# Kernel tuning notes

Hardware: AMD Instinct MI355X
Metric: run time of the kernel (lower is better)

Reference implementation:

```python
import jax, jax.numpy as jnp
import numpy as np

N_NODES = 30000
N_EDGES = 300000
N_TRIP = 200000
NUM_RELS = 8
F_RAW = 128
D = 256  # rgcn_in_dim == h_dim


def setup_inputs() -> dict:
    key = jax.random.key(0)
    ks = jax.random.split(key, 14)
    feats = jax.random.normal(ks[0], (N_NODES, F_RAW), jnp.float32)
    src = jax.random.randint(ks[1], (N_EDGES,), 0, N_NODES)
    dst = jax.random.randint(ks[2], (N_EDGES,), 0, N_NODES)
    etype = jax.random.randint(ks[3], (N_EDGES,), 0, NUM_RELS)
    trip_s = jax.random.randint(ks[4], (N_TRIP,), 0, N_NODES)
    trip_r = jax.random.randint(ks[5], (N_TRIP,), 0, NUM_RELS)
    trip_o = jax.random.randint(ks[6], (N_TRIP,), 0, N_NODES)
    # learned parameters
    W_affine = jax.random.normal(ks[7], (F_RAW, D), jnp.float32) * (1.0 / np.sqrt(F_RAW))
    b_affine = jnp.zeros((D,), jnp.float32)
    W_fwd = jax.random.normal(ks[8], (NUM_RELS, D, D), jnp.float32) * (1.0 / np.sqrt(D))
    W_bwd = jax.random.normal(ks[9], (NUM_RELS, D, D), jnp.float32) * (1.0 / np.sqrt(D))
    W_loop = jax.random.normal(ks[10], (D, D), jnp.float32) * (1.0 / np.sqrt(D))
    w_relation = jax.random.normal(ks[11], (NUM_RELS, D), jnp.float32)  # nn.init.normal_(0,1)
    return {
        "feats": feats, "W_affine": W_affine, "b_affine": b_affine,
        "W_fwd": W_fwd, "W_bwd": W_bwd, "W_loop": W_loop,
        "w_relation": w_relation,
        "src": src, "dst": dst, "etype": etype,
        "trip_s": trip_s, "trip_r": trip_r, "trip_o": trip_o,
    }


def reference(feats, W_affine, b_affine, W_fwd, W_bwd, W_loop, w_relation,
              src, dst, etype, trip_s, trip_r, trip_o):
    # LinearAffine: raw features -> rgcn_in_dim
    x = feats @ W_affine + b_affine                      # [N, D]
    n = x.shape[0]
    # Per-relation transforms of all node features: [R, N, D]
    tf = jnp.einsum('ni,rio->rno', x, W_fwd)
    tb = jnp.einsum('ni,rio->rno', x, W_bwd)
    # Forward-direction messages: gather per-edge transformed src, scatter-add to dst
    msg_f = tf[etype, src]                               # [E, D]
    agg = jnp.zeros((n, x.shape[1]), x.dtype).at[dst].add(msg_f)
    # Backward-direction messages: transformed dst features scattered to src
    msg_b = tb[etype, dst]                               # [E, D]
    agg = agg.at[src].add(msg_b)
    # Self-loop
    h = agg + x @ W_loop                                 # [N, D]
    # DistMult triplet scoring
    s = h[trip_s]
    r = w_relation[trip_r]
    o = h[trip_o]
    weights = jnp.sum(s * r * o, axis=1)                 # [T]
    return weights, h
```

## Files before the change

### kernel.cpp

```cpp
#include <hip/hip_runtime.h>

#define N_NODES 30000
#define N_EDGES 300000
#define N_TRIP 200000
#define NUM_RELS 8
#define F_RAW 128
#define DDIM 256

#define NBUCK (2 * NUM_RELS * N_NODES)
#define SCAN_CHUNK 1024
#define NCHUNK ((NBUCK + SCAN_CHUNK - 1) / SCAN_CHUNK)
#define NPAD (NCHUNK * SCAN_CHUNK)

#define KBIG 2304
#define KBWD 2048
#define KMRG 4352

typedef __attribute__((ext_vector_type(8))) short short8;
typedef __attribute__((ext_vector_type(4))) float f32x4;

__device__ inline unsigned short f2bf(float f) {
  unsigned u = __builtin_bit_cast(unsigned, f);
  u = (u + 0x7FFFu + ((u >> 16) & 1u)) >> 16;
  return (unsigned short)u;
}
__device__ inline float bf2f(unsigned short s) {
  unsigned u = ((unsigned)s) << 16;
  return __builtin_bit_cast(float, u);
}

__global__ void zero_int_kernel(int* __restrict__ p, int n) {
  int i = blockIdx.x * blockDim.x + threadIdx.x;
  if (i < n) p[i] = 0;
}

__global__ void hist_kernel(const int* __restrict__ src,
                            const int* __restrict__ dst,
                            const int* __restrict__ et, int* __restrict__ cnt) {
  int e = blockIdx.x * blockDim.x + threadIdx.x;
  if (e >= N_EDGES) return;
  int r = et[e];
  atomicAdd(&cnt[r * N_NODES + dst[e]], 1);
  atomicAdd(&cnt[(NUM_RELS + r) * N_NODES + src[e]], 1);
}

__global__ __launch_bounds__(256) void scan1_kernel(const int* __restrict__ cnt,
                                                    int* __restrict__ offs,
                                                    int* __restrict__ bsum) {
  __shared__ int s[256];
  const int b = blockIdx.x, t = threadIdx.x;
  const int base = b * SCAN_CHUNK + t * 4;
  int4 v = *reinterpret_cast<const int4*>(&cnt[base]);
  int tsum = v.x + v.y + v.z + v.w;
  s[t] = tsum;
  __syncthreads();
  for (int off = 1; off < 256; off <<= 1) {
    int x = (t >= off) ? s[t - off] : 0;
    __syncthreads();
    s[t] += x;
    __syncthreads();
  }
  int excl = s[t] - tsum;
  offs[base + 0] = excl;
  offs[base + 1] = excl + v.x;
  offs[base + 2] = excl + v.x + v.y;
  offs[base + 3] = excl + v.x + v.y + v.z;
  if (t == 0) bsum[b] = s[255];
}

__global__ __launch_bounds__(512) void scan2_kernel(int* __restrict__ bsum) {
  __shared__ int s[512];
  const int t = threadIdx.x;
  int v = (t < NCHUNK) ? bsum[t] : 0;
  s[t] = v;
  __syncthreads();
  for (int off = 1; off < 512; off <<= 1) {
    int x = (t >= off) ? s[t - off] : 0;
    __syncthreads();
    s[t] += x;
    __syncthreads();
  }
  if (t < NCHUNK) bsum[t] = s[t] - v;
}

__global__ void scan3_kernel(int* __restrict__ offs,
                             const int* __restrict__ bsum,
                             int* __restrict__ cur) {
  int i = blockIdx.x * blockDim.x + threadIdx.x;
  if (i >= NPAD) return;
  int v = offs[i] + bsum[i / SCAN_CHUNK];
  offs[i] = v;
  if (i < NBUCK) cur[i] = v;
}

__global__ void fill_kernel(const int* __restrict__ src,
                            const int* __restrict__ dst,
                            const int* __restrict__ et, int* __restrict__ cur,
                            int* __restrict__ gidx) {
  int e = blockIdx.x * blockDim.x + threadIdx.x;
  if (e >= N_EDGES) return;
  int r = et[e];
  int s = src[e], d = dst[e];
  int p1 = atomicAdd(&cur[r * N_NODES + d], 1);
  gidx[p1] = s;
  int p2 = atomicAdd(&cur[(NUM_RELS + r) * N_NODES + s], 1);
  gidx[p2] = d;
}

__global__ void convert_bf16_kernel(const float* __restrict__ src,
                                    unsigned short* __restrict__ dst,
                                    int total) {
  const int i = blockIdx.x * blockDim.x + threadIdx.x;
  if (i < total) dst[i] = f2bf(src[i]);
}

__global__ void transpose_bf16_kernel(const float* __restrict__ src,
                                      unsigned short* __restrict__ dst,
                                      int R, int K, int N) {
  const int i = blockIdx.x * blockDim.x + threadIdx.x;
  const int total = R * K * N;
  if (i >= total) return;
  const int r = i / (K * N);
  const int rem = i - r * K * N;
  const int k = rem / N;
  const int n = rem - k * N;
  dst[(size_t)r * K * N + (size_t)n * K + k] = f2bf(src[i]);
}

__global__ void build_wcat2_kernel(const float* __restrict__ W8,
                                   const float* __restrict__ Wextra,
                                   unsigned short* __restrict__ dst, int KK) {
  const int i = blockIdx.x * blockDim.x + threadIdx.x;
  if (i >= 256 * KK) return;
  const int n = i / KK;
  const int kk = i - n * KK;
  float v;
  if (kk < 2048) {
    const int r = kk >> 8, k = kk & 255;
    v = W8[((size_t)r * 256 + k) * 256 + n];
  } else {
    v = Wextra[(size_t)(kk - 2048) * 256 + n];
  }
  dst[i] = f2bf(v);
}

__global__ void build_wcat3_kernel(const float* __restrict__ Wf,
                                   const float* __restrict__ Wb,
                                   const float* __restrict__ Wl,
                                   unsigned short* __restrict__ dst) {
  const int i = blockIdx.x * blockDim.x + threadIdx.x;
  if (i >= 256 * KMRG) return;
  const int n = i / KMRG;
  const int kk = i - n * KMRG;
  float v;
  if (kk < 2048) {
    const int r = kk >> 8, k = kk & 255;
    v = Wf[((size_t)r * 256 + k) * 256 + n];
  } else if (kk < 4096) {
    const int r = (kk - 2048) >> 8, k = kk & 255;
    v = Wb[((size_t)r * 256 + k) * 256 + n];
  } else {
    v = Wl[(size_t)(kk - 4096) * 256 + n];
  }
  dst[i] = f2bf(v);
}

template <int OUT_MODE, int ADD_BIAS>
__global__ __launch_bounds__(256) void gemm128_kernel(
    const unsigned short* __restrict__ A, int lda, int K,
    const unsigned short* __restrict__ Bt, const float* __restrict__ bias,
    float* __restrict__ Cf, unsigned short* __restrict__ Cb, int ldc, int M) {
  __shared__ __align__(16) unsigned short As[128 * 64];
  __shared__ __align__(16) unsigned short Bs[128 * 64];

  const int tid = threadIdx.x;
  const int lane = tid & 63;
  const int wave = tid >> 6;
  const int bm = blockIdx.y * 128;
  const int bn = blockIdx.x * 128;
  const int wr = wave >> 1;
  const int wc = wave & 1;
  const int g = lane >> 4;
  const int rl = lane & 15;

  f32x4 acc[4][4];
#pragma unroll
  for (int i = 0; i < 4; ++i)
#pragma unroll
    for (int j = 0; j < 4; ++j) acc[i][j] = (f32x4){0.f, 0.f, 0.f, 0.f};

  for (int k0 = 0; k0 < K; k0 += 64) {
#pragma unroll
    for (int c = 0; c < 8; ++c) {
      const int chunk = c * 4 + wave;
      if (chunk < 16) {
        const int S = chunk * 64 + lane;
        const int row = S >> 3;
        const int s = S & 7;
        int grow = bm + row;
        if (grow > M - 1) grow = M - 1;
        const int kcol = k0 + ((s ^ (row & 7)) << 3);
        const unsigned short* gp = A + (size_t)grow * lda + kcol;
        unsigned short* lp = As + (size_t)chunk * 512;
        __builtin_amdgcn_global_load_lds(
            (const __attribute__((address_space(1))) void*)gp,
            (__attribute__((address_space(3))) void*)lp, 16, 0, 0);
      } else {
        const int S = (chunk - 16) * 64 + lane;
        const int row = S >> 3;
        const int s = S & 7;
        const int kcol = k0 + ((s ^ (row & 7)) << 3);
        const unsigned short* gp = Bt + (size_t)(bn + row) * K + kcol;
        unsigned short* lp = Bs + (size_t)(chunk - 16) * 512;
        __builtin_amdgcn_global_load_lds(
            (const __attribute__((address_space(1))) void*)gp,
            (__attribute__((address_space(3))) void*)lp, 16, 0, 0);
      }
    }
    __syncthreads();

#pragma unroll
    for (int kk = 0; kk < 2; ++kk) {
      short8 a[4], b[4];
#pragma unroll
      for (int mi = 0; mi < 4; ++mi) {
        const int row = wr * 64 + mi * 16 + rl;
        const int slot = (kk * 4 + g) ^ (row & 7);
        a[mi] = *(const short8*)&As[row * 64 + slot * 8];
      }
#pragma unroll
      for (int ni = 0; ni < 4; ++ni) {
        const int row = wc * 64 + ni * 16 + rl;
        const int slot = (kk * 4 + g) ^ (row & 7);
        b[ni] = *(const short8*)&Bs[row * 64 + slot * 8];
      }
#pragma unroll
      for (int mi = 0; mi < 4; ++mi)
#pragma unroll
        for (int ni = 0; ni < 4; ++ni)
          acc[mi][ni] = __builtin_amdgcn_mfma_f32_16x16x32_bf16(
              a[mi], b[ni], acc[mi][ni], 0, 0, 0);
    }
    __syncthreads();
  }

#pragma unroll
  for (int mi = 0; mi < 4; ++mi) {
#pragma unroll
    for (int j = 0; j < 4; ++j) {
      const int row = bm + wr * 64 + mi * 16 + g * 4 + j;
      if (row >= M) continue;
#pragma unroll
      for (int ni = 0; ni < 4; ++ni) {
        const int col = bn + wc * 64 + ni * 16 + rl;
        float v = acc[mi][ni][j];
        if (ADD_BIAS) v += bias[col];
        const size_t idx = (size_t)row * ldc + col;
        if (OUT_MODE == 0) {
          Cf[idx] = v;
        } else if (OUT_MODE == 1) {
          Cb[idx] = f2bf(v);
        } else if (OUT_MODE == 2) {
          v += Cf[idx];
          Cf[idx] = v;
          Cb[idx] = f2bf(v);
        } else {
          Cf[idx] = v;
          Cb[idx] = f2bf(v);
        }
      }
    }
  }
}

__global__ __launch_bounds__(256) void zgather_kernel(
    unsigned short* __restrict__ Z, int ldz, int colbase, int xoff,
    const int* __restrict__ offs_base, const int* __restrict__ gidx) {
  const int b = blockIdx.x * 4 + (threadIdx.x >> 6);
  if (b >= NUM_RELS * N_NODES) return;
  const int lane = threadIdx.x & 63;
  const int r = b / N_NODES;
  const int v = b - r * N_NODES;
  const int s = offs_base[b], e = offs_base[b + 1];

  float ax = 0.f, ay = 0.f, az = 0.f, aw = 0.f;
  for (int i = s; i < e; i += 4) {
    int gq[4];
    ushort4 xs[4];
#pragma unroll
    for (int q = 0; q < 4; ++q)
      if (i + q < e) gq[q] = gidx[i + q];
#pragma unroll
    for (int q = 0; q < 4; ++q)
      if (i + q < e)
        xs[q] = *(const ushort4*)&Z[(size_t)gq[q] * ldz + xoff + lane * 4];
#pragma unroll
    for (int q = 0; q < 4; ++q)
      if (i + q < e) {
        ax += bf2f(xs[q].x);
        ay += bf2f(xs[q].y);
        az += bf2f(xs[q].z);
        aw += bf2f(xs[q].w);
      }
  }
  ushort4 o;
  o.x = f2bf(ax); o.y = f2bf(ay); o.z = f2bf(az); o.w = f2bf(aw);
  *(ushort4*)&Z[(size_t)v * ldz + colbase + r * 256 + lane * 4] = o;
}

__global__ __launch_bounds__(256) void score_bf16_kernel(
    const unsigned short* __restrict__ hb, const float* __restrict__ wrel,
    const int* __restrict__ ts, const int* __restrict__ tr,
    const int* __restrict__ to, float* __restrict__ out, int T) {
  const int t = blockIdx.x * 4 + (threadIdx.x >> 6);
  if (t >= T) return;
  const int lane = threadIdx.x & 63;
  const int s = ts[t];
  const int r = tr[t];
  const int o = to[t];
  const ushort4 hs =
      *reinterpret_cast<const ushort4*>(&hb[(size_t)s * DDIM + lane * 4]);
  const ushort4 ho =
      *reinterpret_cast<const ushort4*>(&hb[(size_t)o * DDIM + lane * 4]);
  const float4 wr =
      *reinterpret_cast<const float4*>(&wrel[(size_t)r * DDIM + lane * 4]);
  float sum = bf2f(hs.x) * wr.x * bf2f(ho.x) + bf2f(hs.y) * wr.y * bf2f(ho.y) +
              bf2f(hs.z) * wr.z * bf2f(ho.z) + bf2f(hs.w) * wr.w * bf2f(ho.w);
#pragma unroll
  for (int off = 32; off; off >>= 1) sum += __shfl_down(sum, off, 64);
  if (lane == 0) out[t] = sum;
}

extern "C" void kernel_launch(void* const* d_in, const int* in_sizes, int n_in,
                              void* d_out, int out_size, void* d_ws,
                              size_t ws_size, hipStream_t stream) {
  const float* feats = (const float*)d_in[0];
  const float* W_affine = (const float*)d_in[1];
  const float* b_affine = (const float*)d_in[2];
  const float* W_fwd = (const float*)d_in[3];
  const float* W_bwd = (const float*)d_in[4];
  const float* W_loop = (const float*)d_in[5];
  const float* w_relation = (const float*)d_in[6];
  const int* src = (const int*)d_in[7];
  const int* dst = (const int*)d_in[8];
  const int* etype = (const int*)d_in[9];
  const int* trip_s = (const int*)d_in[10];
  const int* trip_r = (const int*)d_in[11];
  const int* trip_o = (const int*)d_in[12];

  float* out_w = (float*)d_out;
  float* h = out_w + N_TRIP;

  char* ws = (char*)d_ws;
  const dim3 ggrid(2, (N_NODES + 127) / 128);

  if (ws_size >= 295000000ULL) {
    unsigned short* fb = (unsigned short*)(ws);
    unsigned short* Z = (unsigned short*)(ws + 7680000);
    unsigned short* hbf = (unsigned short*)(ws + 268800000);
    unsigned short* Wta = (unsigned short*)(ws + 284160000);
    unsigned short* Wcat = (unsigned short*)(ws + 284225536);
    int* cnt = (int*)(ws + 286453760);
    int* offs = (int*)(ws + 288374784);
    int* cur = (int*)(ws + 290295808);
    int* bsum = (int*)(ws + 292216832);
    int* gidx = (int*)(ws + 292218880);

    zero_int_kernel<<<(NPAD + 255) / 256, 256, 0, stream>>>(cnt, NPAD);
    hist_kernel<<<(N_EDGES + 255) / 256, 256, 0, stream>>>(src, dst, etype, cnt);
    scan1_kernel<<<NCHUNK, 256, 0, stream>>>(cnt, offs, bsum);
    scan2_kernel<<<1, 512, 0, stream>>>(bsum);
    scan3_kernel<<<(NPAD + 255) / 256, 256, 0, stream>>>(offs, bsum, cur);
    fill_kernel<<<(N_EDGES + 255) / 256, 256, 0, stream>>>(src, dst, etype,
                                                           cur, gidx);

    convert_bf16_kernel<<<(N_NODES * F_RAW + 255) / 256, 256, 0, stream>>>(
        feats, fb, N_NODES * F_RAW);
    transpose_bf16_kernel<<<(F_RAW * DDIM + 255) / 256, 256, 0, stream>>>(
        W_affine, Wta, 1, F_RAW, DDIM);
    build_wcat3_kernel<<<(256 * KMRG + 255) / 256, 256, 0, stream>>>(
        W_fwd, W_bwd, W_loop, Wcat);

    gemm128_kernel<1, 1><<<ggrid, 256, 0, stream>>>(
        fb, F_RAW, F_RAW, Wta, b_affine, nullptr, Z + 4096, KMRG, N_NODES);
    zgather_kernel<<<(NUM_RELS * N_NODES + 3) / 4, 256, 0, stream>>>(
        Z, KMRG, 0, 4096, offs, gidx);
    zgather_kernel<<<(NUM_RELS * N_NODES + 3) / 4, 256, 0, stream>>>(
        Z, KMRG, 2048, 4096, offs + NUM_RELS * N_NODES, gidx);
    gemm128_kernel<3, 0><<<ggrid, 256, 0, stream>>>(
        Z, KMRG, KMRG, Wcat, nullptr, h, hbf, DDIM, N_NODES);

    score_bf16_kernel<<<(N_TRIP + 3) / 4, 256, 0, stream>>>(
        hbf, w_relation, trip_s, trip_r, trip_o, out_w, N_TRIP);
    return;
  }

  unsigned short* fb = (unsigned short*)(ws);
  unsigned short* Z = (unsigned short*)(ws + 7680000);
  unsigned short* hbf = (unsigned short*)(ws + 145920000);
  unsigned short* Wta = (unsigned short*)(ws + 161280000);
  unsigned short* Wcat1 = (unsigned short*)(ws + 161345536);
  unsigned short* Wcat2 = (unsigned short*)(ws + 162525184);
  int* cnt = (int*)(ws + 163573760);
  int* offs = (int*)(ws + 165494784);
  int* cur = (int*)(ws + 167415808);
  int* bsum = (int*)(ws + 169336832);
  int* gidx = (int*)(ws + 169338880);

  zero_int_kernel<<<(NPAD + 255) / 256, 256, 0, stream>>>(cnt, NPAD);
  hist_kernel<<<(N_EDGES + 255) / 256, 256, 0, stream>>>(src, dst, etype, cnt);
  scan1_kernel<<<NCHUNK, 256, 0, stream>>>(cnt, offs, bsum);
  scan2_kernel<<<1, 512, 0, stream>>>(bsum);
  scan3_kernel<<<(NPAD + 255) / 256, 256, 0, stream>>>(offs, bsum, cur);
  fill_kernel<<<(N_EDGES + 255) / 256, 256, 0, stream>>>(src, dst, etype, cur,
                                                         gidx);

  convert_bf16_kernel<<<(N_NODES * F_RAW + 255) / 256, 256, 0, stream>>>(
      feats, fb, N_NODES * F_RAW);
  transpose_bf16_kernel<<<(F_RAW * DDIM + 255) / 256, 256, 0, stream>>>(
      W_affine, Wta, 1, F_RAW, DDIM);
  build_wcat2_kernel<<<(256 * KBIG + 255) / 256, 256, 0, stream>>>(
      W_fwd, W_loop, Wcat1, KBIG);
  build_wcat2_kernel<<<(256 * KBWD + 255) / 256, 256, 0, stream>>>(
      W_bwd, nullptr, Wcat2, KBWD);

  gemm128_kernel<1, 1><<<ggrid, 256, 0, stream>>>(
      fb, F_RAW, F_RAW, Wta, b_affine, nullptr, Z + 2048, KBIG, N_NODES);
  zgather_kernel<<<(NUM_RELS * N_NODES + 3) / 4, 256, 0, stream>>>(
      Z, KBIG, 0, 2048, offs, gidx);
  gemm128_kernel<0, 0><<<ggrid, 256, 0, stream>>>(
      Z, KBIG, KBIG, Wcat1, nullptr, h, nullptr, DDIM, N_NODES);
  zgather_kernel<<<(NUM_RELS * N_NODES + 3) / 4, 256, 0, stream>>>(
      Z, KBIG, 0, 2048, offs + NUM_RELS * N_NODES, gidx);
  gemm128_kernel<2, 0><<<ggrid, 256, 0, stream>>>(
      Z, KBIG, KBWD, Wcat2, nullptr, h, hbf, DDIM, N_NODES);

  score_bf16_kernel<<<(N_TRIP + 3) / 4, 256, 0, stream>>>(
      hbf, w_relation, trip_s, trip_r, trip_o, out_w, N_TRIP);
}
```

Measured before the change: 359.9 us.

## Use 64-row GEMM tiles with XCD-aware remap and 8-wide gather/score

Removes the large-workspace merged path (single K=4352 GEMM) and always uses the two-pass KBIG/KBWD path. The big GEMMs move to a new 64x128 tile kernel that remaps block IDs across the 8 XCDs. The aim is more blocks to fill the CUs and better L2 locality per XCD. The gather and scoring kernels now use 32 lanes per row with 16-byte loads, so each wave handles two rows. The trade-off is less reuse per tile, and if the merged path was active before, the pipeline is now longer.

```diff
diff --git a/kernel.cpp b/kernel.cpp
--- a/kernel.cpp
+++ b/kernel.cpp
@@ -14,9 +14,9 @@
 
 #define KBIG 2304
 #define KBWD 2048
-#define KMRG 4352
 
 typedef __attribute__((ext_vector_type(8))) short short8;
+typedef __attribute__((ext_vector_type(8))) unsigned short u16x8;
 typedef __attribute__((ext_vector_type(4))) float f32x4;
 
 __device__ inline unsigned short f2bf(float f) {
@@ -144,32 +144,10 @@
   dst[i] = f2bf(v);
 }
 
-__global__ void build_wcat3_kernel(const float* __restrict__ Wf,
-                                   const float* __restrict__ Wb,
-                                   const float* __restrict__ Wl,
-                                   unsigned short* __restrict__ dst) {
-  const int i = blockIdx.x * blockDim.x + threadIdx.x;
-  if (i >= 256 * KMRG) return;
-  const int n = i / KMRG;
-  const int kk = i - n * KMRG;
-  float v;
-  if (kk < 2048) {
-    const int r = kk >> 8, k = kk & 255;
-    v = Wf[((size_t)r * 256 + k) * 256 + n];
-  } else if (kk < 4096) {
-    const int r = (kk - 2048) >> 8, k = kk & 255;
-    v = Wb[((size_t)r * 256 + k) * 256 + n];
-  } else {
-    v = Wl[(size_t)(kk - 4096) * 256 + n];
-  }
-  dst[i] = f2bf(v);
-}
-
-template <int OUT_MODE, int ADD_BIAS>
 __global__ __launch_bounds__(256) void gemm128_kernel(
     const unsigned short* __restrict__ A, int lda, int K,
     const unsigned short* __restrict__ Bt, const float* __restrict__ bias,
-    float* __restrict__ Cf, unsigned short* __restrict__ Cb, int ldc, int M) {
+    unsigned short* __restrict__ Cb, int ldc, int M) {
   __shared__ __align__(16) unsigned short As[128 * 64];
   __shared__ __align__(16) unsigned short Bs[128 * 64];
 
@@ -253,82 +231,182 @@
 #pragma unroll
       for (int ni = 0; ni < 4; ++ni) {
         const int col = bn + wc * 64 + ni * 16 + rl;
+        Cb[(size_t)row * ldc + col] = f2bf(acc[mi][ni][j] + bias[col]);
+      }
+    }
+  }
+}
+
+template <int OUT_MODE>
+__global__ __launch_bounds__(256) void gemm64_kernel(
+    const unsigned short* __restrict__ A, int lda, int K,
+    const unsigned short* __restrict__ Bt, float* __restrict__ Cf,
+    unsigned short* __restrict__ Cb, int ldc, int M, int nblk) {
+  __shared__ __align__(16) unsigned short As[64 * 64];
+  __shared__ __align__(16) unsigned short Bs[128 * 64];
+
+  const int tid = threadIdx.x;
+  const int lane = tid & 63;
+  const int wave = tid >> 6;
+
+  const int orig = blockIdx.x;
+  const int q = nblk >> 3, r = nblk & 7;
+  const int xcd = orig & 7, off = orig >> 3;
+  const int wg =
+      (xcd < r) ? xcd * (q + 1) + off : r * (q + 1) + (xcd - r) * q + off;
+  const int bm = (wg >> 1) * 64;
+  const int bn = (wg & 1) * 128;
+
+  const int wr = wave >> 1;
+  const int wc = wave & 1;
+  const int g = lane >> 4;
+  const int rl = lane & 15;
+
+  f32x4 acc[2][4];
+#pragma unroll
+  for (int i = 0; i < 2; ++i)
+#pragma unroll
+    for (int j = 0; j < 4; ++j) acc[i][j] = (f32x4){0.f, 0.f, 0.f, 0.f};
+
+  for (int k0 = 0; k0 < K; k0 += 64) {
+#pragma unroll
+    for (int c = 0; c < 6; ++c) {
+      const int chunk = c * 4 + wave;
+      if (chunk < 8) {
+        const int S = chunk * 64 + lane;
+        const int row = S >> 3;
+        const int s = S & 7;
+        int grow = bm + row;
+        if (grow > M - 1) grow = M - 1;
+        const unsigned short* gp =
+            A + (size_t)grow * lda + k0 + ((s ^ (row & 7)) << 3);
+        unsigned short* lp = As + (size_t)chunk * 512;
+        __builtin_amdgcn_global_load_lds(
+            (const __attribute__((address_space(1))) void*)gp,
+            (__attribute__((address_space(3))) void*)lp, 16, 0, 0);
+      } else {
+        const int S = (chunk - 8) * 64 + lane;
+        const int row = S >> 3;
+        const int s = S & 7;
+        const unsigned short* gp =
+            Bt + (size_t)(bn + row) * K + k0 + ((s ^ (row & 7)) << 3);
+        unsigned short* lp = Bs + (size_t)(chunk - 8) * 512;
+        __builtin_amdgcn_global_load_lds(
+            (const __attribute__((address_space(1))) void*)gp,
+            (__attribute__((address_space(3))) void*)lp, 16, 0, 0);
+      }
+    }
+    __syncthreads();
+
+#pragma unroll
+    for (int kk = 0; kk < 2; ++kk) {
+      short8 a[2], b[4];
+#pragma unroll
+      for (int mi = 0; mi < 2; ++mi) {
+        const int row = wr * 32 + mi * 16 + rl;
+        const int slot = (kk * 4 + g) ^ (row & 7);
+        a[mi] = *(const short8*)&As[row * 64 + slot * 8];
+      }
+#pragma unroll
+      for (int ni = 0; ni < 4; ++ni) {
+        const int row = wc * 64 + ni * 16 + rl;
+        const int slot = (kk * 4 + g) ^ (row & 7);
+        b[ni] = *(const short8*)&Bs[row * 64 + slot * 8];
+      }
+#pragma unroll
+      for (int mi = 0; mi < 2; ++mi)
+#pragma unroll
+        for (int ni = 0; ni < 4; ++ni)
+          acc[mi][ni] = __builtin_amdgcn_mfma_f32_16x16x32_bf16(
+              a[mi], b[ni], acc[mi][ni], 0, 0, 0);
+    }
+    __syncthreads();
+  }
+
+#pragma unroll
+  for (int mi = 0; mi < 2; ++mi) {
+#pragma unroll
+    for (int j = 0; j < 4; ++j) {
+      const int row = bm + wr * 32 + mi * 16 + g * 4 + j;
+      if (row >= M) continue;
+#pragma unroll
+      for (int ni = 0; ni < 4; ++ni) {
+        const int col = bn + wc * 64 + ni * 16 + rl;
         float v = acc[mi][ni][j];
-        if (ADD_BIAS) v += bias[col];
         const size_t idx = (size_t)row * ldc + col;
         if (OUT_MODE == 0) {
           Cf[idx] = v;
-        } else if (OUT_MODE == 1) {
-          Cb[idx] = f2bf(v);
-        } else if (OUT_MODE == 2) {
+        } else {
           v += Cf[idx];
           Cf[idx] = v;
           Cb[idx] = f2bf(v);
-        } else {
-          Cf[idx] = v;
-          Cb[idx] = f2bf(v);
         }
       }
     }
   }
 }
 
-__global__ __launch_bounds__(256) void zgather_kernel(
-    unsigned short* __restrict__ Z, int ldz, int colbase, int xoff,
+__global__ __launch_bounds__(256) void zgatherw_kernel(
+    unsigned short* __restrict__ Z, int colbase,
     const int* __restrict__ offs_base, const int* __restrict__ gidx) {
-  const int b = blockIdx.x * 4 + (threadIdx.x >> 6);
+  const int lane = threadIdx.x & 63;
+  const int hl = lane >> 5;
+  const int l5 = lane & 31;
+  const int b = blockIdx.x * 8 + (threadIdx.x >> 6) * 2 + hl;
   if (b >= NUM_RELS * N_NODES) return;
-  const int lane = threadIdx.x & 63;
   const int r = b / N_NODES;
   const int v = b - r * N_NODES;
   const int s = offs_base[b], e = offs_base[b + 1];
 
-  float ax = 0.f, ay = 0.f, az = 0.f, aw = 0.f;
+  float acc[8] = {};
   for (int i = s; i < e; i += 4) {
-    int gq[4];
-    ushort4 xs[4];
+    int g4[4];
+    u16x8 xs[4];
 #pragma unroll
     for (int q = 0; q < 4; ++q)
-      if (i + q < e) gq[q] = gidx[i + q];
+      if (i + q < e) g4[q] = gidx[i + q];
 #pragma unroll
     for (int q = 0; q < 4; ++q)
       if (i + q < e)
-        xs[q] = *(const ushort4*)&Z[(size_t)gq[q] * ldz + xoff + lane * 4];
+        xs[q] = *(const u16x8*)&Z[(size_t)g4[q] * KBIG + 2048 + l5 * 8];
 #pragma unroll
     for (int q = 0; q < 4; ++q)
       if (i + q < e) {
-        ax += bf2f(xs[q].x);
-        ay += bf2f(xs[q].y);
-        az += bf2f(xs[q].z);
-        aw += bf2f(xs[q].w);
-      }
-  }
-  ushort4 o;
-  o.x = f2bf(ax); o.y = f2bf(ay); o.z = f2bf(az); o.w = f2bf(aw);
-  *(ushort4*)&Z[(size_t)v * ldz + colbase + r * 256 + lane * 4] = o;
-}
-
-__global__ __launch_bounds__(256) void score_bf16_kernel(
+#pragma unroll
+        for (int j = 0; j < 8; ++j) acc[j] += bf2f((unsigned short)xs[q][j]);
+      }
+  }
+  u16x8 o;
+#pragma unroll
+  for (int j = 0; j < 8; ++j) o[j] = (short)f2bf(acc[j]);
+  *(u16x8*)&Z[(size_t)v * KBIG + colbase + r * 256 + l5 * 8] = o;
+}
+
+__global__ __launch_bounds__(256) void score32_kernel(
     const unsigned short* __restrict__ hb, const float* __restrict__ wrel,
     const int* __restrict__ ts, const int* __restrict__ tr,
     const int* __restrict__ to, float* __restrict__ out, int T) {
-  const int t = blockIdx.x * 4 + (threadIdx.x >> 6);
+  const int t = blockIdx.x * 8 + (threadIdx.x >> 5);
   if (t >= T) return;
-  const int lane = threadIdx.x & 63;
+  const int l5 = threadIdx.x & 31;
   const int s = ts[t];
   const int r = tr[t];
   const int o = to[t];
-  const ushort4 hs =
-      *reinterpret_cast<const ushort4*>(&hb[(size_t)s * DDIM + lane * 4]);
-  const ushort4 ho =
-      *reinterpret_cast<const ushort4*>(&hb[(size_t)o * DDIM + lane * 4]);
-  const float4 wr =
-      *reinterpret_cast<const float4*>(&wrel[(size_t)r * DDIM + lane * 4]);
-  float sum = bf2f(hs.x) * wr.x * bf2f(ho.x) + bf2f(hs.y) * wr.y * bf2f(ho.y) +
-              bf2f(hs.z) * wr.z * bf2f(ho.z) + bf2f(hs.w) * wr.w * bf2f(ho.w);
-#pragma unroll
-  for (int off = 32; off; off >>= 1) sum += __shfl_down(sum, off, 64);
-  if (lane == 0) out[t] = sum;
+  const u16x8 hs = *(const u16x8*)&hb[(size_t)s * DDIM + l5 * 8];
+  const u16x8 ho = *(const u16x8*)&hb[(size_t)o * DDIM + l5 * 8];
+  const float4 w0 = *(const float4*)&wrel[(size_t)r * DDIM + l5 * 8];
+  const float4 w1 = *(const float4*)&wrel[(size_t)r * DDIM + l5 * 8 + 4];
+  float sum = bf2f((unsigned short)hs[0]) * w0.x * bf2f((unsigned short)ho[0]) +
+              bf2f((unsigned short)hs[1]) * w0.y * bf2f((unsigned short)ho[1]) +
+              bf2f((unsigned short)hs[2]) * w0.z * bf2f((unsigned short)ho[2]) +
+              bf2f((unsigned short)hs[3]) * w0.w * bf2f((unsigned short)ho[3]) +
+              bf2f((unsigned short)hs[4]) * w1.x * bf2f((unsigned short)ho[4]) +
+              bf2f((unsigned short)hs[5]) * w1.y * bf2f((unsigned short)ho[5]) +
+              bf2f((unsigned short)hs[6]) * w1.z * bf2f((unsigned short)ho[6]) +
+              bf2f((unsigned short)hs[7]) * w1.w * bf2f((unsigned short)ho[7]);
+#pragma unroll
+  for (int off = 16; off; off >>= 1) sum += __shfl_down(sum, off, 32);
+  if (l5 == 0) out[t] = sum;
 }
 
 extern "C" void kernel_launch(void* const* d_in, const int* in_sizes, int n_in,
@@ -352,49 +430,6 @@
   float* h = out_w + N_TRIP;
 
   char* ws = (char*)d_ws;
-  const dim3 ggrid(2, (N_NODES + 127) / 128);
-
-  if (ws_size >= 295000000ULL) {
-    unsigned short* fb = (unsigned short*)(ws);
-    unsigned short* Z = (unsigned short*)(ws + 7680000);
-    unsigned short* hbf = (unsigned short*)(ws + 268800000);
-    unsigned short* Wta = (unsigned short*)(ws + 284160000);
-    unsigned short* Wcat = (unsigned short*)(ws + 284225536);
-    int* cnt = (int*)(ws + 286453760);
-    int* offs = (int*)(ws + 288374784);
-    int* cur = (int*)(ws + 290295808);
-    int* bsum = (int*)(ws + 292216832);
-    int* gidx = (int*)(ws + 292218880);
-
-    zero_int_kernel<<<(NPAD + 255) / 256, 256, 0, stream>>>(cnt, NPAD);
-    hist_kernel<<<(N_EDGES + 255) / 256, 256, 0, stream>>>(src, dst, etype, cnt);
-    scan1_kernel<<<NCHUNK, 256, 0, stream>>>(cnt, offs, bsum);
-    scan2_kernel<<<1, 512, 0, stream>>>(bsum);
-    scan3_kernel<<<(NPAD + 255) / 256, 256, 0, stream>>>(offs, bsum, cur);
-    fill_kernel<<<(N_EDGES + 255) / 256, 256, 0, stream>>>(src, dst, etype,
-                                                           cur, gidx);
-
-    convert_bf16_kernel<<<(N_NODES * F_RAW + 255) / 256, 256, 0, stream>>>(
-        feats, fb, N_NODES * F_RAW);
-    transpose_bf16_kernel<<<(F_RAW * DDIM + 255) / 256, 256, 0, stream>>>(
-        W_affine, Wta, 1, F_RAW, DDIM);
-    build_wcat3_kernel<<<(256 * KMRG + 255) / 256, 256, 0, stream>>>(
-        W_fwd, W_bwd, W_loop, Wcat);
-
-    gemm128_kernel<1, 1><<<ggrid, 256, 0, stream>>>(
-        fb, F_RAW, F_RAW, Wta, b_affine, nullptr, Z + 4096, KMRG, N_NODES);
-    zgather_kernel<<<(NUM_RELS * N_NODES + 3) / 4, 256, 0, stream>>>(
-        Z, KMRG, 0, 4096, offs, gidx);
-    zgather_kernel<<<(NUM_RELS * N_NODES + 3) / 4, 256, 0, stream>>>(
-        Z, KMRG, 2048, 4096, offs + NUM_RELS * N_NODES, gidx);
-    gemm128_kernel<3, 0><<<ggrid, 256, 0, stream>>>(
-        Z, KMRG, KMRG, Wcat, nullptr, h, hbf, DDIM, N_NODES);
-
-    score_bf16_kernel<<<(N_TRIP + 3) / 4, 256, 0, stream>>>(
-        hbf, w_relation, trip_s, trip_r, trip_o, out_w, N_TRIP);
-    return;
-  }
-
   unsigned short* fb = (unsigned short*)(ws);
   unsigned short* Z = (unsigned short*)(ws + 7680000);
   unsigned short* hbf = (unsigned short*)(ws + 145920000);
@@ -424,17 +459,21 @@
   build_wcat2_kernel<<<(256 * KBWD + 255) / 256, 256, 0, stream>>>(
       W_bwd, nullptr, Wcat2, KBWD);
 
-  gemm128_kernel<1, 1><<<ggrid, 256, 0, stream>>>(
-      fb, F_RAW, F_RAW, Wta, b_affine, nullptr, Z + 2048, KBIG, N_NODES);
-  zgather_kernel<<<(NUM_RELS * N_NODES + 3) / 4, 256, 0, stream>>>(
-      Z, KBIG, 0, 2048, offs, gidx);
-  gemm128_kernel<0, 0><<<ggrid, 256, 0, stream>>>(
-      Z, KBIG, KBIG, Wcat1, nullptr, h, nullptr, DDIM, N_NODES);
-  zgather_kernel<<<(NUM_RELS * N_NODES + 3) / 4, 256, 0, stream>>>(
-      Z, KBIG, 0, 2048, offs + NUM_RELS * N_NODES, gidx);
-  gemm128_kernel<2, 0><<<ggrid, 256, 0, stream>>>(
-      Z, KBIG, KBWD, Wcat2, nullptr, h, hbf, DDIM, N_NODES);
-
-  score_bf16_kernel<<<(N_TRIP + 3) / 4, 256, 0, stream>>>(
+  const dim3 agrid(2, (N_NODES + 127) / 128);
+  gemm128_kernel<<<agrid, 256, 0, stream>>>(fb, F_RAW, F_RAW, Wta, b_affine,
+                                            Z + 2048, KBIG, N_NODES);
+
+  const int nblk = 2 * ((N_NODES + 63) / 64);
+  const int zgrid = (NUM_RELS * N_NODES + 7) / 8;
+
+  zgatherw_kernel<<<zgrid, 256, 0, stream>>>(Z, 0, offs, gidx);
+  gemm64_kernel<0><<<nblk, 256, 0, stream>>>(Z, KBIG, KBIG, Wcat1, h, nullptr,
+                                             DDIM, N_NODES, nblk);
+  zgatherw_kernel<<<zgrid, 256, 0, stream>>>(Z, 0, offs + NUM_RELS * N_NODES,
+                                             gidx);
+  gemm64_kernel<2><<<nblk, 256, 0, stream>>>(Z, KBIG, KBWD, Wcat2, h, hbf,
+                                             DDIM, N_NODES, nblk);
+
+  score32_kernel<<<(N_TRIP + 7) / 8, 256, 0, stream>>>(
       hbf, w_relation, trip_s, trip_r, trip_o, out_w, N_TRIP);
 }
```

Measured after the change: 298.1 us. 1.21x faster.
